# Kernel tuning notes

Measured on AMD Instinct MI355X. Metric: run time of the kernel, lower is better.

Reference implementation:

```python
import jax, jax.numpy as jnp
import numpy as np

EMB = 1024
HEADS = 16
HEAD_DIM = EMB // HEADS

def setup_inputs() -> dict:
    key = jax.random.key(0)
    ks = jax.random.split(key, 12)
    s = 0.02
    x = jax.random.normal(ks[0], (2, 2048, EMB), dtype=jnp.float32)
    return {
        "x": x,
        "wq": jax.random.normal(ks[1], (EMB, EMB), jnp.float32) * s,
        "bq": jnp.zeros((EMB,), jnp.float32),
        "wk": jax.random.normal(ks[2], (EMB, EMB), jnp.float32) * s,
        "bk": jnp.zeros((EMB,), jnp.float32),
        "wv": jax.random.normal(ks[3], (EMB, EMB), jnp.float32) * s,
        "bv": jnp.zeros((EMB,), jnp.float32),
        "wo": jax.random.normal(ks[4], (EMB, EMB), jnp.float32) * s,
        "bo": jnp.zeros((EMB,), jnp.float32),
        "gamma": jnp.ones((EMB,), jnp.float32),
        "beta": jnp.zeros((EMB,), jnp.float32),
    }

def _layernorm(x, gamma, beta, eps=1e-5):
    mu = jnp.mean(x, axis=-1, keepdims=True)
    var = jnp.mean(jnp.square(x - mu), axis=-1, keepdims=True)
    return (x - mu) * jax.lax.rsqrt(var + eps) * gamma + beta

def reference(x, wq, bq, wk, bk, wv, bv, wo, bo, gamma, beta):
    B, T, D = x.shape
    H, d_k = HEADS, HEAD_DIM
    # Linear(y = x W^T + b), then split heads
    q = (x @ wq.T + bq).reshape(B, T, H, d_k)
    k = (x @ wk.T + bk).reshape(B, T, H, d_k)
    v = (x @ wv.T + bv).reshape(B, T, H, d_k)
    scores = jnp.einsum('bthd,bshd->bhts', q, k) / jnp.sqrt(jnp.float32(d_k))
    attn = jax.nn.softmax(scores, axis=-1)  # dropout is identity in eval mode
    out = jnp.einsum('bhts,bshd->bthd', attn, v).reshape(B, T, D)
    out = out @ wo.T + bo
    return _layernorm(x + out, gamma, beta)
```

## Files before the change

kernel.cpp:

```cpp
#include <hip/hip_runtime.h>
#include <stdint.h>
#include <stddef.h>


typedef __bf16 bf16_t;
typedef bf16_t bf16x8 __attribute__((ext_vector_type(8)));
typedef float f32x4 __attribute__((ext_vector_type(4)));
typedef uint16_t u16x8 __attribute__((ext_vector_type(8)));

#define MFMA(a, b, c) __builtin_amdgcn_mfma_f32_16x16x32_bf16((a), (b), (c), 0, 0, 0)

__device__ __forceinline__ uint16_t f2bf(float f) {
  __bf16 h = (__bf16)f;
  return *(uint16_t*)&h;
}

__device__ __forceinline__ void gload16(const void* g, void* l) {
  __builtin_amdgcn_global_load_lds((const __attribute__((address_space(1))) void*)g,
                                   (__attribute__((address_space(3))) void*)l,
                                   16, 0, 0);
}

__global__ __launch_bounds__(256) void cvt_all(
    const float* __restrict__ x, const float* __restrict__ wq,
    const float* __restrict__ wk, const float* __restrict__ wv,
    const float* __restrict__ wo, uint16_t* __restrict__ xb,
    uint16_t* __restrict__ wqb, uint16_t* __restrict__ wkb,
    uint16_t* __restrict__ wvb, uint16_t* __restrict__ wob) {
  const int gid = blockIdx.x * 256 + threadIdx.x;
  const float* src; uint16_t* dst; int off;
  if (gid < 1048576) {
    src = x; dst = xb; off = gid;
  } else {
    const int t = gid - 1048576;
    off = t & 262143;
    switch (t >> 18) {
      case 0: src = wq; dst = wqb; break;
      case 1: src = wk; dst = wkb; break;
      case 2: src = wv; dst = wvb; break;
      default: src = wo; dst = wob; break;
    }
  }
  const float4 f = ((const float4*)src)[off];
  uint64_t p = (uint64_t)f2bf(f.x) | ((uint64_t)f2bf(f.y) << 16) |
               ((uint64_t)f2bf(f.z) << 32) | ((uint64_t)f2bf(f.w) << 48);
  ((uint64_t*)dst)[off] = p;
}

template <bool OUT_BF16>
__device__ __forceinline__ void gemm128(const uint16_t* __restrict__ A,
                                        const uint16_t* __restrict__ Bt,
                                        const float* __restrict__ bias,
                                        float oscale,
                                        uint16_t* __restrict__ outb,
                                        float* __restrict__ outf) {
  __shared__ uint16_t sA[2][128 * 32];
  __shared__ uint16_t sB[2][128 * 32];
  const int tid = threadIdx.x;
  const int lane = tid & 63, w = tid >> 6;
  const int quad = lane >> 4, l15 = lane & 15;
  const int m0 = blockIdx.y * 128, n0 = blockIdx.x * 128;
  const int wm = (w >> 1) * 64, wn = (w & 1) * 64;

  const int ch0 = tid, ch1 = tid + 256;
  const int r0 = ch0 >> 2, g0 = (((ch0 & 3) ^ (r0 & 3)) << 3);
  const int r1 = ch1 >> 2, g1 = (((ch1 & 3) ^ (r1 & 3)) << 3);
  const uint16_t* a0 = A + (size_t)(m0 + r0) * 1024 + g0;
  const uint16_t* a1 = A + (size_t)(m0 + r1) * 1024 + g1;
  const uint16_t* b0 = Bt + (size_t)(n0 + r0) * 1024 + g0;
  const uint16_t* b1 = Bt + (size_t)(n0 + r1) * 1024 + g1;

  gload16(a0, &sA[0][ch0 * 8]);
  gload16(a1, &sA[0][ch1 * 8]);
  gload16(b0, &sB[0][ch0 * 8]);
  gload16(b1, &sB[0][ch1 * 8]);

  f32x4 acc[4][4] = {};

  for (int kt = 0; kt < 32; ++kt) {
    __syncthreads();
    const int cur = kt & 1;
    if (kt < 31) {
      const int ko = (kt + 1) * 32;
      const int nxt = cur ^ 1;
      gload16(a0 + ko, &sA[nxt][ch0 * 8]);
      gload16(a1 + ko, &sA[nxt][ch1 * 8]);
      gload16(b0 + ko, &sB[nxt][ch0 * 8]);
      gload16(b1 + ko, &sB[nxt][ch1 * 8]);
    }
    bf16x8 af[4], bfr[4];
#pragma unroll
    for (int i = 0; i < 4; ++i) {
      const int row = wm + i * 16 + l15;
      af[i] = *(const bf16x8*)&sA[cur][row * 32 + ((quad ^ (row & 3)) << 3)];
    }
#pragma unroll
    for (int j = 0; j < 4; ++j) {
      const int row = wn + j * 16 + l15;
      bfr[j] = *(const bf16x8*)&sB[cur][row * 32 + ((quad ^ (row & 3)) << 3)];
    }
#pragma unroll
    for (int i = 0; i < 4; ++i)
#pragma unroll
      for (int j = 0; j < 4; ++j) acc[i][j] = MFMA(af[i], bfr[j], acc[i][j]);
  }

#pragma unroll
  for (int i = 0; i < 4; ++i) {
#pragma unroll
    for (int j = 0; j < 4; ++j) {
      const int gm = m0 + wm + i * 16 + quad * 4;
      const int gn = n0 + wn + j * 16 + l15;
      const float bv = bias[gn];
#pragma unroll
      for (int r = 0; r < 4; ++r) {
        const float v = (acc[i][j][r] + bv) * oscale;
        const size_t idx = (size_t)(gm + r) * 1024 + gn;
        if constexpr (OUT_BF16) outb[idx] = f2bf(v);
        else outf[idx] = v;
      }
    }
  }
}

#define QSCALE 0.18033688011112042f

__global__ __launch_bounds__(256) void qkv_gemm(
    const uint16_t* __restrict__ xb, const uint16_t* __restrict__ wqb,
    const uint16_t* __restrict__ wkb, const uint16_t* __restrict__ wvb,
    const float* __restrict__ bq, const float* __restrict__ bk,
    const float* __restrict__ bv, uint16_t* __restrict__ qb,
    uint16_t* __restrict__ kb, uint16_t* __restrict__ vb) {
  const uint16_t* Bt; const float* bias; uint16_t* out; float sc;
  if (blockIdx.z == 0)      { Bt = wqb; bias = bq; out = qb; sc = QSCALE; }
  else if (blockIdx.z == 1) { Bt = wkb; bias = bk; out = kb; sc = 1.f; }
  else                      { Bt = wvb; bias = bv; out = vb; sc = 1.f; }
  gemm128<true>(xb, Bt, bias, sc, out, nullptr);
}

__global__ __launch_bounds__(256) void o_gemm(const uint16_t* __restrict__ ab,
                                              const uint16_t* __restrict__ wob,
                                              const float* __restrict__ bo,
                                              float* __restrict__ y) {
  gemm128<false>(ab, wob, bo, 1.f, nullptr, y);
}

__global__ __launch_bounds__(256) void v_trans(const uint16_t* __restrict__ vb,
                                               uint16_t* __restrict__ vbT) {
  __shared__ uint16_t sT[64 * 136];
  const int tid = threadIdx.x;
  const int t0 = blockIdx.x * 128;
  const int h = blockIdx.y, b = blockIdx.z;
#pragma unroll
  for (int c = 0; c < 4; ++c) {
    const int idx = c * 256 + tid;
    const int t = idx >> 3, d8 = (idx & 7) * 8;
    u16x8 v = *(const u16x8*)&vb[(size_t)(b * 2048 + t0 + t) * 1024 + h * 64 + d8];
#pragma unroll
    for (int e = 0; e < 8; ++e) sT[(d8 + e) * 136 + t] = v[e];
  }
  __syncthreads();
  const size_t obase = ((size_t)(b * 16 + h) * 64) * 2048 + t0;
#pragma unroll
  for (int c = 0; c < 4; ++c) {
    const int idx = c * 256 + tid;
    const int d = idx >> 4, t8 = (idx & 15) * 8;
    u16x8 v = *(const u16x8*)&sT[d * 136 + t8];
    *(u16x8*)&vbT[obase + (size_t)d * 2048 + t8] = v;
  }
}

__global__ __launch_bounds__(512) void attn(const uint16_t* __restrict__ qb,
                                            const uint16_t* __restrict__ kb,
                                            const uint16_t* __restrict__ vbT,
                                            uint16_t* __restrict__ ab) {
  __shared__ uint16_t sK[2][64 * 64];
  __shared__ uint16_t sV[2][64 * 64];
  __shared__ uint16_t sP[128 * 72];
  const int tid = threadIdx.x;
  const int lane = tid & 63, w = tid >> 6;
  const int quad = lane >> 4, l15 = lane & 15;
  const int hb = blockIdx.x;
  const int h = hb & 15, b = hb >> 4;
  const int q0 = blockIdx.y * 128;
  const size_t qkbase = (size_t)b * 2048 * 1024 + (size_t)h * 64;
  const size_t vtbase = (size_t)hb * 64 * 2048;

  const int sr = tid >> 3, sp = tid & 7, sg = ((sp ^ (sr & 7)) << 3);
  const uint16_t* kAd = kb + qkbase + (size_t)sr * 1024 + sg;
  const uint16_t* vAd = vbT + vtbase + (size_t)sr * 2048 + sg;

  gload16(kAd, &sK[0][tid * 8]);
  gload16(vAd, &sV[0][tid * 8]);

  bf16x8 qa[2];
  {
    const uint16_t* qrow =
        qb + qkbase + (size_t)(q0 + w * 16 + l15) * 1024 + quad * 8;
    qa[0] = *(const bf16x8*)(qrow);
    qa[1] = *(const bf16x8*)(qrow + 32);
  }

  f32x4 acc_o[4] = {};
  float li[4] = {0.f, 0.f, 0.f, 0.f};

  for (int kt = 0; kt < 32; ++kt) {
    __syncthreads();
    const int cur = kt & 1;
    if (kt < 31) {
      const int so = (kt + 1) * 64;
      gload16(kAd + (size_t)so * 1024, &sK[cur ^ 1][tid * 8]);
      gload16(vAd + so, &sV[cur ^ 1][tid * 8]);
    }

    f32x4 acc_s[4] = {};
#pragma unroll
    for (int ks = 0; ks < 2; ++ks) {
#pragma unroll
      for (int j = 0; j < 4; ++j) {
        const int brow = j * 16 + l15;
        const bf16x8 bb =
            *(const bf16x8*)&sK[cur][brow * 64 + (((ks * 4 + quad) ^ (brow & 7)) << 3)];
        acc_s[j] = MFMA(qa[ks], bb, acc_s[j]);
      }
    }

    __bf16* sPb = (__bf16*)sP;
#pragma unroll
    for (int r = 0; r < 4; ++r) {
      const int prow = w * 16 + quad * 4 + r;
      float rsum = li[r];
#pragma unroll
      for (int j = 0; j < 4; ++j) {
        const float p = __builtin_amdgcn_exp2f(acc_s[j][r]);
        rsum += p;
        sPb[prow * 72 + j * 16 + l15] = (__bf16)p;
      }
      li[r] = rsum;
    }

#pragma unroll
    for (int ks2 = 0; ks2 < 2; ++ks2) {
      const int prow = w * 16 + l15;
      const bf16x8 pa = *(const bf16x8*)&sP[prow * 72 + ks2 * 32 + quad * 8];
#pragma unroll
      for (int jo = 0; jo < 4; ++jo) {
        const int vrow = jo * 16 + l15;
        const bf16x8 vv =
            *(const bf16x8*)&sV[cur][vrow * 64 + (((ks2 * 4 + quad) ^ (vrow & 7)) << 3)];
        acc_o[jo] = MFMA(pa, vv, acc_o[jo]);
      }
    }
  }

#pragma unroll
  for (int r = 0; r < 4; ++r) {
    float s = li[r];
#pragma unroll
    for (int o = 1; o < 16; o <<= 1) s += __shfl_xor(s, o);
    li[r] = 1.f / s;
  }

#pragma unroll
  for (int jo = 0; jo < 4; ++jo)
#pragma unroll
    for (int r = 0; r < 4; ++r) {
      const int row = q0 + w * 16 + quad * 4 + r;
      const int col = h * 64 + jo * 16 + l15;
      ab[(size_t)(b * 2048 + row) * 1024 + col] = f2bf(acc_o[jo][r] * li[r]);
    }
}

__global__ __launch_bounds__(256) void resid_ln(const float* __restrict__ x,
                                                const float* __restrict__ y,
                                                const float* __restrict__ gamma,
                                                const float* __restrict__ beta,
                                                float* __restrict__ out) {
  const int row = blockIdx.x, tid = threadIdx.x;
  const size_t base = (size_t)row * 1024 + tid * 4;
  const float4 xv = *(const float4*)(x + base);
  const float4 yv = *(const float4*)(y + base);
  const float a = xv.x + yv.x, b2 = xv.y + yv.y, c = xv.z + yv.z, d = xv.w + yv.w;
  float s = a + b2 + c + d;
#pragma unroll
  for (int o = 1; o < 64; o <<= 1) s += __shfl_xor(s, o);
  __shared__ float red[4];
  const int w = tid >> 6;
  if ((tid & 63) == 0) red[w] = s;
  __syncthreads();
  const float mu = (red[0] + red[1] + red[2] + red[3]) * (1.f / 1024.f);
  const float da = a - mu, db = b2 - mu, dc = c - mu, dd = d - mu;
  float sq = da * da + db * db + dc * dc + dd * dd;
#pragma unroll
  for (int o = 1; o < 64; o <<= 1) sq += __shfl_xor(sq, o);
  __syncthreads();
  if ((tid & 63) == 0) red[w] = sq;
  __syncthreads();
  const float var = (red[0] + red[1] + red[2] + red[3]) * (1.f / 1024.f);
  const float rs = rsqrtf(var + 1e-5f);
  const float4 g = *(const float4*)(gamma + tid * 4);
  const float4 bt = *(const float4*)(beta + tid * 4);
  float4 o4;
  o4.x = da * rs * g.x + bt.x;
  o4.y = db * rs * g.y + bt.y;
  o4.z = dc * rs * g.z + bt.z;
  o4.w = dd * rs * g.w + bt.w;
  *(float4*)(out + base) = o4;
}

extern "C" void kernel_launch(void* const* d_in, const int* in_sizes, int n_in,
                              void* d_out, int out_size, void* d_ws, size_t ws_size,
                              hipStream_t stream) {
  const float* x     = (const float*)d_in[0];
  const float* wq    = (const float*)d_in[1];
  const float* bq    = (const float*)d_in[2];
  const float* wk    = (const float*)d_in[3];
  const float* bk    = (const float*)d_in[4];
  const float* wv    = (const float*)d_in[5];
  const float* bv    = (const float*)d_in[6];
  const float* wo    = (const float*)d_in[7];
  const float* bo    = (const float*)d_in[8];
  const float* gamma = (const float*)d_in[9];
  const float* beta  = (const float*)d_in[10];
  float* out = (float*)d_out;
  char* ws = (char*)d_ws;
  const size_t MB = 1024 * 1024;
  uint16_t* xb  = (uint16_t*)(ws);
  uint16_t* ab  = xb;
  uint16_t* wqb = (uint16_t*)(ws + 8 * MB);
  uint16_t* wkb = (uint16_t*)(ws + 10 * MB);
  uint16_t* wvb = (uint16_t*)(ws + 12 * MB);
  uint16_t* wob = (uint16_t*)(ws + 14 * MB);
  uint16_t* qb  = (uint16_t*)(ws + 16 * MB);
  uint16_t* kb  = (uint16_t*)(ws + 24 * MB);
  uint16_t* vb  = (uint16_t*)(ws + 32 * MB);
  uint16_t* vbT = (uint16_t*)(ws + 40 * MB);
  float*    y   = (float*)(ws + 16 * MB);

  cvt_all<<<8192, 256, 0, stream>>>(x, wq, wk, wv, wo, xb, wqb, wkb, wvb, wob);
  qkv_gemm<<<dim3(8, 32, 3), 256, 0, stream>>>(xb, wqb, wkb, wvb, bq, bk, bv, qb, kb, vb);
  v_trans<<<dim3(16, 16, 2), 256, 0, stream>>>(vb, vbT);
  attn<<<dim3(32, 16), 512, 0, stream>>>(qb, kb, vbT, ab);
  o_gemm<<<dim3(8, 32), 256, 0, stream>>>(ab, wob, bo, y);
  resid_ln<<<4096, 256, 0, stream>>>(x, y, gamma, beta, out);
}
```

Baseline: 227.5 us.

## Switch GEMM and attention to 32x32x16 MFMA with 32-row warp tiles

Replaces the 16x16x32 bf16 MFMA with the 32x32x16 variant in both the shared GEMM routine and the attention kernel. In the GEMM each warp now computes a 2x2 grid of 32x32 tiles, and the LDS fragment loads and output index mapping are rewritten to match. Attention drops to 256 threads, with each warp owning 32 query rows, a per-warp swizzled P buffer, and two K/V loads per thread. The larger MFMA tiles are meant to cut LDS fragment traffic and instruction count per FLOP, at the cost of more accumulator registers per thread and fewer waves per attention block.

```diff
diff --git a/kernel.cpp b/kernel.cpp
--- a/kernel.cpp
+++ b/kernel.cpp
@@ -5,10 +5,10 @@
 
 typedef __bf16 bf16_t;
 typedef bf16_t bf16x8 __attribute__((ext_vector_type(8)));
-typedef float f32x4 __attribute__((ext_vector_type(4)));
+typedef float f32x16 __attribute__((ext_vector_type(16)));
 typedef uint16_t u16x8 __attribute__((ext_vector_type(8)));
 
-#define MFMA(a, b, c) __builtin_amdgcn_mfma_f32_16x16x32_bf16((a), (b), (c), 0, 0, 0)
+#define MFMA32(a, b, c) __builtin_amdgcn_mfma_f32_32x32x16_bf16((a), (b), (c), 0, 0, 0)
 
 __device__ __forceinline__ uint16_t f2bf(float f) {
   __bf16 h = (__bf16)f;
@@ -58,7 +58,7 @@
   __shared__ uint16_t sB[2][128 * 32];
   const int tid = threadIdx.x;
   const int lane = tid & 63, w = tid >> 6;
-  const int quad = lane >> 4, l15 = lane & 15;
+  const int l31 = lane & 31, half = lane >> 5;
   const int m0 = blockIdx.y * 128, n0 = blockIdx.x * 128;
   const int wm = (w >> 1) * 64, wn = (w & 1) * 64;
 
@@ -75,7 +75,7 @@
   gload16(b0, &sB[0][ch0 * 8]);
   gload16(b1, &sB[0][ch1 * 8]);
 
-  f32x4 acc[4][4] = {};
+  f32x16 acc[2][2] = {};
 
   for (int kt = 0; kt < 32; ++kt) {
     __syncthreads();
@@ -88,34 +88,38 @@
       gload16(b0 + ko, &sB[nxt][ch0 * 8]);
       gload16(b1 + ko, &sB[nxt][ch1 * 8]);
     }
-    bf16x8 af[4], bfr[4];
-#pragma unroll
-    for (int i = 0; i < 4; ++i) {
-      const int row = wm + i * 16 + l15;
-      af[i] = *(const bf16x8*)&sA[cur][row * 32 + ((quad ^ (row & 3)) << 3)];
-    }
-#pragma unroll
-    for (int j = 0; j < 4; ++j) {
-      const int row = wn + j * 16 + l15;
-      bfr[j] = *(const bf16x8*)&sB[cur][row * 32 + ((quad ^ (row & 3)) << 3)];
-    }
-#pragma unroll
-    for (int i = 0; i < 4; ++i)
-#pragma unroll
-      for (int j = 0; j < 4; ++j) acc[i][j] = MFMA(af[i], bfr[j], acc[i][j]);
-  }
-
-#pragma unroll
-  for (int i = 0; i < 4; ++i) {
-#pragma unroll
-    for (int j = 0; j < 4; ++j) {
-      const int gm = m0 + wm + i * 16 + quad * 4;
-      const int gn = n0 + wn + j * 16 + l15;
+#pragma unroll
+    for (int s = 0; s < 2; ++s) {
+      const int c = s * 2 + half;
+      bf16x8 af[2], bfr[2];
+#pragma unroll
+      for (int i = 0; i < 2; ++i) {
+        const int arow = wm + i * 32 + l31;
+        af[i] = *(const bf16x8*)&sA[cur][arow * 32 + ((c ^ (arow & 3)) << 3)];
+      }
+#pragma unroll
+      for (int j = 0; j < 2; ++j) {
+        const int brow = wn + j * 32 + l31;
+        bfr[j] = *(const bf16x8*)&sB[cur][brow * 32 + ((c ^ (brow & 3)) << 3)];
+      }
+#pragma unroll
+      for (int i = 0; i < 2; ++i)
+#pragma unroll
+        for (int j = 0; j < 2; ++j) acc[i][j] = MFMA32(af[i], bfr[j], acc[i][j]);
+    }
+  }
+
+#pragma unroll
+  for (int i = 0; i < 2; ++i) {
+#pragma unroll
+    for (int j = 0; j < 2; ++j) {
+      const int gn = n0 + wn + j * 32 + l31;
       const float bv = bias[gn];
 #pragma unroll
-      for (int r = 0; r < 4; ++r) {
-        const float v = (acc[i][j][r] + bv) * oscale;
-        const size_t idx = (size_t)(gm + r) * 1024 + gn;
+      for (int reg = 0; reg < 16; ++reg) {
+        const int gm = m0 + wm + i * 32 + (reg & 3) + 8 * (reg >> 2) + 4 * half;
+        const float v = (acc[i][j][reg] + bv) * oscale;
+        const size_t idx = (size_t)gm * 1024 + gn;
         if constexpr (OUT_BF16) outb[idx] = f2bf(v);
         else outf[idx] = v;
       }
@@ -170,104 +174,118 @@
   }
 }
 
-__global__ __launch_bounds__(512) void attn(const uint16_t* __restrict__ qb,
+__global__ __launch_bounds__(256) void attn(const uint16_t* __restrict__ qb,
                                             const uint16_t* __restrict__ kb,
                                             const uint16_t* __restrict__ vbT,
                                             uint16_t* __restrict__ ab) {
   __shared__ uint16_t sK[2][64 * 64];
   __shared__ uint16_t sV[2][64 * 64];
-  __shared__ uint16_t sP[128 * 72];
+  __shared__ uint16_t sP[4][32 * 64];
   const int tid = threadIdx.x;
   const int lane = tid & 63, w = tid >> 6;
-  const int quad = lane >> 4, l15 = lane & 15;
+  const int l31 = lane & 31, half = lane >> 5;
   const int hb = blockIdx.x;
   const int h = hb & 15, b = hb >> 4;
   const int q0 = blockIdx.y * 128;
   const size_t qkbase = (size_t)b * 2048 * 1024 + (size_t)h * 64;
   const size_t vtbase = (size_t)hb * 64 * 2048;
 
-  const int sr = tid >> 3, sp = tid & 7, sg = ((sp ^ (sr & 7)) << 3);
-  const uint16_t* kAd = kb + qkbase + (size_t)sr * 1024 + sg;
-  const uint16_t* vAd = vbT + vtbase + (size_t)sr * 2048 + sg;
-
-  gload16(kAd, &sK[0][tid * 8]);
-  gload16(vAd, &sV[0][tid * 8]);
-
-  bf16x8 qa[2];
+  const int ch0 = tid, ch1 = tid + 256;
+  const int r0 = ch0 >> 3, g0 = (((ch0 & 7) ^ (r0 & 7)) << 3);
+  const int r1 = ch1 >> 3, g1 = (((ch1 & 7) ^ (r1 & 7)) << 3);
+  const uint16_t* k0 = kb + qkbase + (size_t)r0 * 1024 + g0;
+  const uint16_t* k1 = kb + qkbase + (size_t)r1 * 1024 + g1;
+  const uint16_t* v0 = vbT + vtbase + (size_t)r0 * 2048 + g0;
+  const uint16_t* v1 = vbT + vtbase + (size_t)r1 * 2048 + g1;
+
+  gload16(k0, &sK[0][ch0 * 8]);
+  gload16(k1, &sK[0][ch1 * 8]);
+  gload16(v0, &sV[0][ch0 * 8]);
+  gload16(v1, &sV[0][ch1 * 8]);
+
+  bf16x8 qa[4];
   {
     const uint16_t* qrow =
-        qb + qkbase + (size_t)(q0 + w * 16 + l15) * 1024 + quad * 8;
-    qa[0] = *(const bf16x8*)(qrow);
-    qa[1] = *(const bf16x8*)(qrow + 32);
-  }
-
-  f32x4 acc_o[4] = {};
-  float li[4] = {0.f, 0.f, 0.f, 0.f};
+        qb + qkbase + (size_t)(q0 + w * 32 + l31) * 1024 + half * 8;
+#pragma unroll
+    for (int s = 0; s < 4; ++s) qa[s] = *(const bf16x8*)(qrow + s * 16);
+  }
+
+  f32x16 acc_o[2] = {};
+  float li[16];
+#pragma unroll
+  for (int r = 0; r < 16; ++r) li[r] = 0.f;
+
+  uint16_t* sPw = sP[w];
+  __bf16* sPb = (__bf16*)sPw;
 
   for (int kt = 0; kt < 32; ++kt) {
     __syncthreads();
     const int cur = kt & 1;
     if (kt < 31) {
-      const int so = (kt + 1) * 64;
-      gload16(kAd + (size_t)so * 1024, &sK[cur ^ 1][tid * 8]);
-      gload16(vAd + so, &sV[cur ^ 1][tid * 8]);
-    }
-
-    f32x4 acc_s[4] = {};
-#pragma unroll
-    for (int ks = 0; ks < 2; ++ks) {
-#pragma unroll
-      for (int j = 0; j < 4; ++j) {
-        const int brow = j * 16 + l15;
-        const bf16x8 bb =
-            *(const bf16x8*)&sK[cur][brow * 64 + (((ks * 4 + quad) ^ (brow & 7)) << 3)];
-        acc_s[j] = MFMA(qa[ks], bb, acc_s[j]);
-      }
-    }
-
-    __bf16* sPb = (__bf16*)sP;
-#pragma unroll
-    for (int r = 0; r < 4; ++r) {
-      const int prow = w * 16 + quad * 4 + r;
-      float rsum = li[r];
-#pragma unroll
-      for (int j = 0; j < 4; ++j) {
-        const float p = __builtin_amdgcn_exp2f(acc_s[j][r]);
-        rsum += p;
-        sPb[prow * 72 + j * 16 + l15] = (__bf16)p;
-      }
-      li[r] = rsum;
-    }
-
-#pragma unroll
-    for (int ks2 = 0; ks2 < 2; ++ks2) {
-      const int prow = w * 16 + l15;
-      const bf16x8 pa = *(const bf16x8*)&sP[prow * 72 + ks2 * 32 + quad * 8];
-#pragma unroll
-      for (int jo = 0; jo < 4; ++jo) {
-        const int vrow = jo * 16 + l15;
+      const size_t so = (size_t)(kt + 1) * 64;
+      const int nxt = cur ^ 1;
+      gload16(k0 + so * 1024, &sK[nxt][ch0 * 8]);
+      gload16(k1 + so * 1024, &sK[nxt][ch1 * 8]);
+      gload16(v0 + so, &sV[nxt][ch0 * 8]);
+      gload16(v1 + so, &sV[nxt][ch1 * 8]);
+    }
+
+    f32x16 acc_s[2] = {};
+#pragma unroll
+    for (int s = 0; s < 4; ++s) {
+      const int c = s * 2 + half;
+#pragma unroll
+      for (int n = 0; n < 2; ++n) {
+        const int brow = n * 32 + l31;
+        const bf16x8 kk =
+            *(const bf16x8*)&sK[cur][brow * 64 + ((c ^ (brow & 7)) << 3)];
+        acc_s[n] = MFMA32(qa[s], kk, acc_s[n]);
+      }
+    }
+
+#pragma unroll
+    for (int reg = 0; reg < 16; ++reg) {
+      const int row = (reg & 3) + 8 * (reg >> 2) + 4 * half;
+#pragma unroll
+      for (int n = 0; n < 2; ++n) {
+        const float p = __builtin_amdgcn_exp2f(acc_s[n][reg]);
+        li[reg] += p;
+        const int col = n * 32 + l31;
+        sPb[row * 64 + (((col >> 3) ^ (row & 7)) << 3) + (col & 7)] = (__bf16)p;
+      }
+    }
+
+#pragma unroll
+    for (int s = 0; s < 4; ++s) {
+      const int c = s * 2 + half;
+      const bf16x8 pa =
+          *(const bf16x8*)&sPw[l31 * 64 + ((c ^ (l31 & 7)) << 3)];
+#pragma unroll
+      for (int n = 0; n < 2; ++n) {
+        const int vrow = n * 32 + l31;
         const bf16x8 vv =
-            *(const bf16x8*)&sV[cur][vrow * 64 + (((ks2 * 4 + quad) ^ (vrow & 7)) << 3)];
-        acc_o[jo] = MFMA(pa, vv, acc_o[jo]);
-      }
-    }
-  }
-
-#pragma unroll
-  for (int r = 0; r < 4; ++r) {
-    float s = li[r];
-#pragma unroll
-    for (int o = 1; o < 16; o <<= 1) s += __shfl_xor(s, o);
-    li[r] = 1.f / s;
-  }
-
-#pragma unroll
-  for (int jo = 0; jo < 4; ++jo)
-#pragma unroll
-    for (int r = 0; r < 4; ++r) {
-      const int row = q0 + w * 16 + quad * 4 + r;
-      const int col = h * 64 + jo * 16 + l15;
-      ab[(size_t)(b * 2048 + row) * 1024 + col] = f2bf(acc_o[jo][r] * li[r]);
+            *(const bf16x8*)&sV[cur][vrow * 64 + ((c ^ (vrow & 7)) << 3)];
+        acc_o[n] = MFMA32(pa, vv, acc_o[n]);
+      }
+    }
+  }
+
+#pragma unroll
+  for (int reg = 0; reg < 16; ++reg) {
+    float s = li[reg];
+#pragma unroll
+    for (int o = 1; o < 32; o <<= 1) s += __shfl_xor(s, o);
+    li[reg] = 1.f / s;
+  }
+
+#pragma unroll
+  for (int n = 0; n < 2; ++n)
+#pragma unroll
+    for (int reg = 0; reg < 16; ++reg) {
+      const int row = q0 + w * 32 + (reg & 3) + 8 * (reg >> 2) + 4 * half;
+      const int col = h * 64 + n * 32 + l31;
+      ab[(size_t)(b * 2048 + row) * 1024 + col] = f2bf(acc_o[n][reg] * li[reg]);
     }
 }
 
@@ -340,7 +358,7 @@
   cvt_all<<<8192, 256, 0, stream>>>(x, wq, wk, wv, wo, xb, wqb, wkb, wvb, wob);
   qkv_gemm<<<dim3(8, 32, 3), 256, 0, stream>>>(xb, wqb, wkb, wvb, bq, bk, bv, qb, kb, vb);
   v_trans<<<dim3(16, 16, 2), 256, 0, stream>>>(vb, vbT);
-  attn<<<dim3(32, 16), 512, 0, stream>>>(qb, kb, vbT, ab);
+  attn<<<dim3(32, 16), 256, 0, stream>>>(qb, kb, vbT, ab);
   o_gemm<<<dim3(8, 32), 256, 0, stream>>>(ab, wob, bo, y);
   resid_ln<<<4096, 256, 0, stream>>>(x, y, gamma, beta, out);
 }
```

Result: no change. 226.2 us (-0.6%).
